# Kernel tuning notes

Hardware: AMD Instinct MI355X
Metric: run time of the kernel (lower is better)

Reference implementation:

```python
import jax, jax.numpy as jnp
import numpy as np

BETA = 0.1


def setup_inputs() -> dict:
    key = jax.random.key(0)
    ks = jax.random.split(key, 8)
    B, S, H, V = 4, 512, 2048, 32000
    return {
        "lin_weight": jax.random.normal(ks[0], (V, H), jnp.float32) * 0.02,
        "_input": jax.random.normal(ks[1], (B, S, H), jnp.float32),
        "attention_mask": jnp.ones((B, S), jnp.float32),
        "rewards": jax.random.normal(ks[2], (B,), jnp.float32),
        "bias": jax.random.normal(ks[3], (V,), jnp.float32) * 0.02,
        "ref_input": jax.random.normal(ks[4], (B, S, H), jnp.float32),
        "ref_weight": jax.random.normal(ks[5], (V, H), jnp.float32) * 0.02,
        "ref_bias": jax.random.normal(ks[6], (V,), jnp.float32) * 0.02,
    }


def _seq_logps(x, w, b, mask):
    # logits: [B,S,V]; per-token max log-softmax, masked, summed over seq
    logits = jnp.einsum("bsh,vh->bsv", x, w) + b
    lp = jax.nn.log_softmax(logits, axis=-1)
    seq = (jnp.max(lp, axis=-1) * mask).sum(axis=-1)  # [B]
    return logits, seq


def reference(lin_weight, _input, attention_mask, rewards, bias, ref_input, ref_weight, ref_bias):
    policy_logits, seq_log_probs = _seq_logps(_input, lin_weight, bias, attention_mask)
    _, ref_seq_logps = _seq_logps(ref_input, ref_weight, ref_bias, attention_mask)
    ref_seq_logps = jax.lax.stop_gradient(ref_seq_logps)

    adv = rewards - rewards.mean()
    std = jnp.std(rewards, ddof=1)  # torch unbiased std
    adv = jnp.where(std > 0, adv / std, adv)

    kl_div = seq_log_probs - ref_seq_logps
    loss = (-(adv * seq_log_probs) + BETA * kl_div).mean()

    metrics = (
        seq_log_probs.mean(),
        jnp.std(seq_log_probs, ddof=1),
        policy_logits.mean(),
        kl_div.mean(),
    )
    return (loss,) + metrics
```

## Files before the change

kernel.cpp:

```cpp
#include <hip/hip_runtime.h>
#include <hip/hip_fp16.h>
#include <math.h>

#define TOK 2048
#define HD 2048
#define VOC 32000
#define BM 256
#define BN 256
#define BK 64
#define NT (HD/BK)
#define NCH (VOC/64)
#define NBLK ((TOK/BM)*(VOC/BN))

typedef _Float16 half8 __attribute__((ext_vector_type(8)));
typedef float float4v __attribute__((ext_vector_type(4)));

#define GLB __attribute__((address_space(1)))
#define LDSAS __attribute__((address_space(3)))

static __device__ __forceinline__ void gload_lds16(const void* g, void* l) {
  __builtin_amdgcn_global_load_lds((const GLB unsigned int*)g,
                                   (LDSAS unsigned int*)l, 16, 0, 0);
}

__global__ void cvt_f32_f16(const float* __restrict__ in,
                            _Float16* __restrict__ out, int n8) {
  for (int i = blockIdx.x * blockDim.x + threadIdx.x; i < n8;
       i += gridDim.x * blockDim.x) {
    float4v a = *(const float4v*)(in + (size_t)i*8);
    float4v b = *(const float4v*)(in + (size_t)i*8 + 4);
    half8 h;
    #pragma unroll
    for (int j=0;j<4;j++) { h[j] = (_Float16)a[j]; h[4+j] = (_Float16)b[j]; }
    *(half8*)(out + (size_t)i*8) = h;
  }
}

template<int CB, bool SG01, bool SG23, int VMN>
__device__ __forceinline__ void ktile(
    unsigned char* ldsby, const char* Xb, const char* Wb,
    int sA0, int sA1, int sB0, int sB1, int ldst0, int ldst1, int kbn,
    const int (&aofs)[2][8], const int (&bofs)[2][4], float4v (&acc)[8][4])
{
  constexpr int BI = CB ? 1 : 0;
  half8 af[4], bf[4];

  #pragma unroll
  for (int m=0;m<4;m++) af[m] = *(const half8*)(ldsby + aofs[BI][m]);
  #pragma unroll
  for (int n=0;n<4;n++) bf[n] = *(const half8*)(ldsby + bofs[BI][n] + 16384);
  if (SG01) {
    gload_lds16(Xb + (sA0 + kbn + 64), ldsby + ((CB^65536) + 32768) + ldst0);
    gload_lds16(Xb + (sA1 + kbn + 64), ldsby + ((CB^65536) + 32768) + ldst1);
  }
  __builtin_amdgcn_s_barrier();
  asm volatile("s_waitcnt lgkmcnt(0)" ::: "memory");
  __builtin_amdgcn_sched_barrier(0);
  __builtin_amdgcn_s_setprio(1);
  #pragma unroll
  for (int m=0;m<4;m++)
    #pragma unroll
    for (int n=0;n<4;n++)
      acc[m][n] = __builtin_amdgcn_mfma_f32_16x16x32_f16(af[m], bf[n], acc[m][n],0,0,0);
  __builtin_amdgcn_s_setprio(0);
  __builtin_amdgcn_s_barrier();

  #pragma unroll
  for (int m=0;m<4;m++) af[m] = *(const half8*)(ldsby + aofs[BI][4+m]);
  if (SG01) {
    gload_lds16(Wb + (sB0 + kbn + 64), ldsby + ((CB^65536) + 49152) + ldst0);
    gload_lds16(Wb + (sB1 + kbn + 64), ldsby + ((CB^65536) + 49152) + ldst1);
  }
  __builtin_amdgcn_s_barrier();
  asm volatile("s_waitcnt lgkmcnt(0)" ::: "memory");
  __builtin_amdgcn_sched_barrier(0);
  __builtin_amdgcn_s_setprio(1);
  #pragma unroll
  for (int m=0;m<4;m++)
    #pragma unroll
    for (int n=0;n<4;n++)
      acc[4+m][n] = __builtin_amdgcn_mfma_f32_16x16x32_f16(af[m], bf[n], acc[4+m][n],0,0,0);
  __builtin_amdgcn_s_setprio(0);
  __builtin_amdgcn_s_barrier();

  #pragma unroll
  for (int m=0;m<4;m++) af[m] = *(const half8*)(ldsby + aofs[BI][m] + 32768);
  #pragma unroll
  for (int n=0;n<4;n++) bf[n] = *(const half8*)(ldsby + bofs[BI][n] + 49152);
  if (SG23) {
    gload_lds16(Xb + (sA0 + kbn + 128), ldsby + (CB + 0) + ldst0);
    gload_lds16(Xb + (sA1 + kbn + 128), ldsby + (CB + 0) + ldst1);
  }
  __builtin_amdgcn_s_barrier();
  asm volatile("s_waitcnt lgkmcnt(0)" ::: "memory");
  __builtin_amdgcn_sched_barrier(0);
  __builtin_amdgcn_s_setprio(1);
  #pragma unroll
  for (int m=0;m<4;m++)
    #pragma unroll
    for (int n=0;n<4;n++)
      acc[m][n] = __builtin_amdgcn_mfma_f32_16x16x32_f16(af[m], bf[n], acc[m][n],0,0,0);
  __builtin_amdgcn_s_setprio(0);
  __builtin_amdgcn_s_barrier();

  #pragma unroll
  for (int m=0;m<4;m++) af[m] = *(const half8*)(ldsby + aofs[BI][4+m] + 32768);
  if (SG23) {
    gload_lds16(Wb + (sB0 + kbn + 128), ldsby + (CB + 16384) + ldst0);
    gload_lds16(Wb + (sB1 + kbn + 128), ldsby + (CB + 16384) + ldst1);
  }
  __builtin_amdgcn_s_barrier();
  asm volatile("s_waitcnt lgkmcnt(0)" ::: "memory");
  __builtin_amdgcn_sched_barrier(0);
  __builtin_amdgcn_s_setprio(1);
  #pragma unroll
  for (int m=0;m<4;m++)
    #pragma unroll
    for (int n=0;n<4;n++)
      acc[4+m][n] = __builtin_amdgcn_mfma_f32_16x16x32_f16(af[m], bf[n], acc[4+m][n],0,0,0);
  __builtin_amdgcn_s_setprio(0);
  if (VMN >= 0) {
    if (VMN == 4) asm volatile("s_waitcnt vmcnt(4)" ::: "memory");
    else          asm volatile("s_waitcnt vmcnt(0)" ::: "memory");
  }
  __builtin_amdgcn_s_barrier();
}

__global__ __launch_bounds__(512, 2) void gemm_stats_f16(
    const _Float16* __restrict__ Xh, const _Float16* __restrict__ Wh,
    const float* __restrict__ bias,
    float* __restrict__ pmax, float* __restrict__ psum,
    float* __restrict__ bsum, int computeSum)
{
  __shared__ unsigned char ldsbuf[131072];
  unsigned char* ldsby = ldsbuf;

  int bid = blockIdx.x;
  int swz = (bid & 7) * (NBLK/8) + (bid >> 3);
  int rowt = swz & 7;
  int colt = swz >> 3;
  int brow = rowt * BM;
  int bcol = colt * BN;

  int tid  = threadIdx.x;
  int lane = tid & 63;
  int wv   = tid >> 6;
  int wr   = wv >> 2;
  int wc   = wv & 3;
  int l15  = lane & 15;
  int q    = lane >> 4;

  int aofs[2][8], bofs[2][4];
  #pragma unroll
  for (int m = 0; m < 8; m++) {
    int r = wr*128 + m*16 + l15;
    int o = r*64 + (((q + r + (r>>2)) & 3) << 4);
    aofs[0][m] = o; aofs[1][m] = o + 65536;
  }
  #pragma unroll
  for (int n = 0; n < 4; n++) {
    int r = wc*64 + n*16 + l15;
    int o = r*64 + (((q + r + (r>>2)) & 3) << 4);
    bofs[0][n] = o; bofs[1][n] = o + 65536;
  }

  int r0 = tid >> 2, c0 = tid & 3;
  int r1 = r0 + 128;
  int q0 = (c0 - r0 - (r0>>2)) & 3;
  int q1 = (c0 - r1 - (r1>>2)) & 3;
  int sA0 = (brow + r0)*(HD*2) + (q0<<4);
  int sA1 = (brow + r1)*(HD*2) + (q1<<4);
  int sB0 = (bcol + r0)*(HD*2) + (q0<<4);
  int sB1 = (bcol + r1)*(HD*2) + (q1<<4);
  int ldst0 = (wv<<10);
  int ldst1 = (wv<<10) + 8192;

  const char* Xb = (const char*)Xh;
  const char* Wb = (const char*)Wh;

  float4v acc[8][4];
  #pragma unroll
  for (int m=0;m<8;m++)
    #pragma unroll
    for (int n=0;n<4;n++) acc[m][n] = (float4v){0.f,0.f,0.f,0.f};

  gload_lds16(Xb + sA0,       ldsby + 0     + ldst0);
  gload_lds16(Xb + sA1,       ldsby + 0     + ldst1);
  gload_lds16(Wb + sB0,       ldsby + 16384 + ldst0);
  gload_lds16(Wb + sB1,       ldsby + 16384 + ldst1);
  gload_lds16(Xb + (sA0+64),  ldsby + 32768 + ldst0);
  gload_lds16(Xb + (sA1+64),  ldsby + 32768 + ldst1);
  gload_lds16(Wb + (sB0+64),  ldsby + 49152 + ldst0);
  gload_lds16(Wb + (sB1+64),  ldsby + 49152 + ldst1);
  gload_lds16(Xb + (sA0+128), ldsby + 65536 + ldst0);
  gload_lds16(Xb + (sA1+128), ldsby + 65536 + ldst1);
  gload_lds16(Wb + (sB0+128), ldsby + 81920 + ldst0);
  gload_lds16(Wb + (sB1+128), ldsby + 81920 + ldst1);
  asm volatile("s_waitcnt vmcnt(4)" ::: "memory");
  __builtin_amdgcn_s_barrier();

  int kbn = 128;
  #pragma unroll 1
  for (int i = 0; i < 15; ++i) {
    ktile<0,     true, true, 4>(ldsby, Xb, Wb, sA0,sA1,sB0,sB1, ldst0,ldst1, kbn, aofs, bofs, acc);
    kbn += 128;
    ktile<65536, true, true, 4>(ldsby, Xb, Wb, sA0,sA1,sB0,sB1, ldst0,ldst1, kbn, aofs, bofs, acc);
    kbn += 128;
  }
  ktile<0,     true,  false, 0>(ldsby, Xb, Wb, sA0,sA1,sB0,sB1, ldst0,ldst1, kbn, aofs, bofs, acc);
  kbn += 128;
  ktile<65536, false, false, -2>(ldsby, Xb, Wb, sA0,sA1,sB0,sB1, ldst0,ldst1, kbn, aofs, bofs, acc);

  float bv[4];
  #pragma unroll
  for (int n=0;n<4;n++) bv[n] = bias[bcol + wc*64 + n*16 + l15];

  float lsum = 0.f;
  int ch = colt*4 + wc;
  #pragma unroll
  for (int m=0;m<8;m++) {
    #pragma unroll
    for (int r=0;r<4;r++) {
      float v0 = acc[m][0][r] + bv[0];
      float v1 = acc[m][1][r] + bv[1];
      float v2 = acc[m][2][r] + bv[2];
      float v3 = acc[m][3][r] + bv[3];
      if (computeSum) lsum += v0+v1+v2+v3;
      float mx = fmaxf(fmaxf(v0,v1), fmaxf(v2,v3));
      #pragma unroll
      for (int off=1; off<16; off<<=1) mx = fmaxf(mx, __shfl_xor(mx, off, 64));
      float se = __expf(v0-mx)+__expf(v1-mx)+__expf(v2-mx)+__expf(v3-mx);
      #pragma unroll
      for (int off=1; off<16; off<<=1) se += __shfl_xor(se, off, 64);
      if (l15 == 0) {
        int row = brow + wr*128 + m*16 + (lane>>4)*4 + r;
        pmax[(size_t)row*NCH + ch] = mx;
        psum[(size_t)row*NCH + ch] = se;
      }
    }
  }

  if (computeSum) {
    #pragma unroll
    for (int off=1; off<64; off<<=1) lsum += __shfl_xor(lsum, off, 64);
    __syncthreads();
    float* red = (float*)ldsbuf;
    if (lane == 0) red[wv] = lsum;
    __syncthreads();
    if (tid == 0) {
      float s = 0.f;
      for (int w=0; w<8; w++) s += red[w];
      bsum[blockIdx.x] = s;
    }
  }
}

__global__ void row_combine(const float* __restrict__ pmax,
                            const float* __restrict__ psum,
                            const float* __restrict__ mask,
                            float* __restrict__ tok)
{
  int row = blockIdx.x;
  int lane = threadIdx.x;
  float M = -INFINITY;
  for (int c = lane; c < NCH; c += 64) M = fmaxf(M, pmax[(size_t)row*NCH + c]);
  #pragma unroll
  for (int off=1; off<64; off<<=1) M = fmaxf(M, __shfl_xor(M, off, 64));
  float L = 0.f;
  for (int c = lane; c < NCH; c += 64)
    L += psum[(size_t)row*NCH + c] * __expf(pmax[(size_t)row*NCH + c] - M);
  #pragma unroll
  for (int off=1; off<64; off<<=1) L += __shfl_xor(L, off, 64);
  if (lane == 0) tok[row] = -logf(L) * mask[row];
}

__global__ void finalize(const float* __restrict__ tokP,
                         const float* __restrict__ tokR,
                         const float* __restrict__ rewards,
                         const float* __restrict__ bsum, int nbsum,
                         float* __restrict__ out)
{
  __shared__ float red[256];
  __shared__ float seqP[4], seqR[4];
  int t = threadIdx.x;
  for (int b=0; b<4; b++) {
    float v = tokP[b*512 + t] + tokP[b*512 + 256 + t];
    red[t] = v; __syncthreads();
    for (int s=128; s>0; s>>=1) { if (t < s) red[t] += red[t+s]; __syncthreads(); }
    if (t == 0) seqP[b] = red[0];
    __syncthreads();
    v = tokR[b*512 + t] + tokR[b*512 + 256 + t];
    red[t] = v; __syncthreads();
    for (int s=128; s>0; s>>=1) { if (t < s) red[t] += red[t+s]; __syncthreads(); }
    if (t == 0) seqR[b] = red[0];
    __syncthreads();
  }
  float ls = 0.f;
  for (int i=t; i<nbsum; i+=256) ls += bsum[i];
  red[t] = ls; __syncthreads();
  for (int s=128; s>0; s>>=1) { if (t < s) red[t] += red[t+s]; __syncthreads(); }
  if (t == 0) {
    float r0=rewards[0], r1=rewards[1], r2=rewards[2], r3=rewards[3];
    float rm = (r0+r1+r2+r3)*0.25f;
    float var = ((r0-rm)*(r0-rm)+(r1-rm)*(r1-rm)+(r2-rm)*(r2-rm)+(r3-rm)*(r3-rm))/3.f;
    float rstd = sqrtf(var);
    float adv[4] = {r0-rm, r1-rm, r2-rm, r3-rm};
    if (rstd > 0.f) { for (int b=0;b<4;b++) adv[b] /= rstd; }
    float loss=0.f, sm=0.f, km=0.f;
    for (int b=0;b<4;b++) {
      float kl = seqP[b] - seqR[b];
      loss += -(adv[b]*seqP[b]) + 0.1f*kl;
      sm += seqP[b]; km += kl;
    }
    loss *= 0.25f; sm *= 0.25f; km *= 0.25f;
    float sv = 0.f;
    for (int b=0;b<4;b++) { float d = seqP[b]-sm; sv += d*d; }
    float sstd = sqrtf(sv/3.f);
    out[0] = loss;
    out[1] = sm;
    out[2] = sstd;
    out[3] = red[0] / ((float)TOK * (float)VOC);
    out[4] = km;
  }
}

extern "C" void kernel_launch(void* const* d_in, const int* in_sizes, int n_in,
                              void* d_out, int out_size, void* d_ws, size_t ws_size,
                              hipStream_t stream) {
  const float* W    = (const float*)d_in[0];
  const float* X    = (const float*)d_in[1];
  const float* mask = (const float*)d_in[2];
  const float* rew  = (const float*)d_in[3];
  const float* bias = (const float*)d_in[4];
  const float* Xr   = (const float*)d_in[5];
  const float* Wr   = (const float*)d_in[6];
  const float* br   = (const float*)d_in[7];
  float* out = (float*)d_out;

  float* pmax = (float*)d_ws;
  float* psum = pmax + (size_t)TOK*NCH;
  float* tokP = psum + (size_t)TOK*NCH;
  float* tokR = tokP + TOK;
  float* bsum = tokR + TOK;

  size_t headFloats = (size_t)TOK*NCH*2 + TOK*2 + 4096;
  size_t offXh = headFloats * 4;
  _Float16* Xh = (_Float16*)((unsigned char*)d_ws + offXh);
  _Float16* Wh = (_Float16*)((unsigned char*)d_ws + offXh + (size_t)TOK*HD*2);

  cvt_f32_f16<<<2048, 256, 0, stream>>>(X,  Xh, TOK*HD/8);
  cvt_f32_f16<<<2048, 256, 0, stream>>>(W,  Wh, VOC*HD/8);
  gemm_stats_f16<<<NBLK, 512, 0, stream>>>(Xh, Wh, bias, pmax, psum, bsum, 1);
  row_combine<<<TOK, 64, 0, stream>>>(pmax, psum, mask, tokP);
  cvt_f32_f16<<<2048, 256, 0, stream>>>(Xr, Xh, TOK*HD/8);
  cvt_f32_f16<<<2048, 256, 0, stream>>>(Wr, Wh, VOC*HD/8);
  gemm_stats_f16<<<NBLK, 512, 0, stream>>>(Xh, Wh, br, pmax, psum, bsum, 0);
  row_combine<<<TOK, 64, 0, stream>>>(pmax, psum, mask, tokR);
  finalize<<<1, 256, 0, stream>>>(tokP, tokR, rew, bsum, NBLK, out);
}
```

Baseline: 718.1 us.

## Merge k-tile GEMM phases into two and overlap LDS reads with MFMAs

Each 128-wide k-step of the fused GEMM now runs in two phases instead of four. All eight A fragments are read from LDS at once, and each phase issues both the X and W prefetches into the other buffer. A partial `lgkmcnt(4)` wait lets the first half of the MFMAs start while the remaining LDS reads are still in flight. This cuts the number of workgroup barriers per k-step and the idle time around them, at the cost of 16 more VGPRs for the extra A fragments, which could raise register pressure under the 512-thread, 2-block launch bound.

```diff
diff --git a/kernel.cpp b/kernel.cpp
--- a/kernel.cpp
+++ b/kernel.cpp
@@ -36,29 +36,37 @@
   }
 }
 
-template<int CB, bool SG01, bool SG23, int VMN>
+template<int CB, bool SG1, bool SG2, int VMN>
 __device__ __forceinline__ void ktile(
     unsigned char* ldsby, const char* Xb, const char* Wb,
     int sA0, int sA1, int sB0, int sB1, int ldst0, int ldst1, int kbn,
     const int (&aofs)[2][8], const int (&bofs)[2][4], float4v (&acc)[8][4])
 {
   constexpr int BI = CB ? 1 : 0;
-  half8 af[4], bf[4];
-
-  #pragma unroll
-  for (int m=0;m<4;m++) af[m] = *(const half8*)(ldsby + aofs[BI][m]);
+  half8 af[8], bf[4];
+
   #pragma unroll
   for (int n=0;n<4;n++) bf[n] = *(const half8*)(ldsby + bofs[BI][n] + 16384);
-  if (SG01) {
+  #pragma unroll
+  for (int m=0;m<8;m++) af[m] = *(const half8*)(ldsby + aofs[BI][m]);
+  if (SG1) {
     gload_lds16(Xb + (sA0 + kbn + 64), ldsby + ((CB^65536) + 32768) + ldst0);
     gload_lds16(Xb + (sA1 + kbn + 64), ldsby + ((CB^65536) + 32768) + ldst1);
-  }
-  __builtin_amdgcn_s_barrier();
+    gload_lds16(Wb + (sB0 + kbn + 64), ldsby + ((CB^65536) + 49152) + ldst0);
+    gload_lds16(Wb + (sB1 + kbn + 64), ldsby + ((CB^65536) + 49152) + ldst1);
+  }
+  asm volatile("s_waitcnt lgkmcnt(4)" ::: "memory");
+  __builtin_amdgcn_sched_barrier(0);
+  __builtin_amdgcn_s_setprio(1);
+  #pragma unroll
+  for (int m=0;m<4;m++)
+    #pragma unroll
+    for (int n=0;n<4;n++)
+      acc[m][n] = __builtin_amdgcn_mfma_f32_16x16x32_f16(af[m], bf[n], acc[m][n],0,0,0);
   asm volatile("s_waitcnt lgkmcnt(0)" ::: "memory");
   __builtin_amdgcn_sched_barrier(0);
-  __builtin_amdgcn_s_setprio(1);
-  #pragma unroll
-  for (int m=0;m<4;m++)
+  #pragma unroll
+  for (int m=4;m<8;m++)
     #pragma unroll
     for (int n=0;n<4;n++)
       acc[m][n] = __builtin_amdgcn_mfma_f32_16x16x32_f16(af[m], bf[n], acc[m][n],0,0,0);
@@ -66,63 +74,33 @@
   __builtin_amdgcn_s_barrier();
 
   #pragma unroll
-  for (int m=0;m<4;m++) af[m] = *(const half8*)(ldsby + aofs[BI][4+m]);
-  if (SG01) {
-    gload_lds16(Wb + (sB0 + kbn + 64), ldsby + ((CB^65536) + 49152) + ldst0);
-    gload_lds16(Wb + (sB1 + kbn + 64), ldsby + ((CB^65536) + 49152) + ldst1);
-  }
-  __builtin_amdgcn_s_barrier();
+  for (int n=0;n<4;n++) bf[n] = *(const half8*)(ldsby + bofs[BI][n] + 49152);
+  #pragma unroll
+  for (int m=0;m<8;m++) af[m] = *(const half8*)(ldsby + aofs[BI][m] + 32768);
+  if (SG2) {
+    gload_lds16(Xb + (sA0 + kbn + 128), ldsby + (CB + 0)     + ldst0);
+    gload_lds16(Xb + (sA1 + kbn + 128), ldsby + (CB + 0)     + ldst1);
+    gload_lds16(Wb + (sB0 + kbn + 128), ldsby + (CB + 16384) + ldst0);
+    gload_lds16(Wb + (sB1 + kbn + 128), ldsby + (CB + 16384) + ldst1);
+  }
+  asm volatile("s_waitcnt lgkmcnt(4)" ::: "memory");
+  __builtin_amdgcn_sched_barrier(0);
+  __builtin_amdgcn_s_setprio(1);
+  #pragma unroll
+  for (int m=0;m<4;m++)
+    #pragma unroll
+    for (int n=0;n<4;n++)
+      acc[m][n] = __builtin_amdgcn_mfma_f32_16x16x32_f16(af[m], bf[n], acc[m][n],0,0,0);
   asm volatile("s_waitcnt lgkmcnt(0)" ::: "memory");
   __builtin_amdgcn_sched_barrier(0);
-  __builtin_amdgcn_s_setprio(1);
-  #pragma unroll
-  for (int m=0;m<4;m++)
-    #pragma unroll
-    for (int n=0;n<4;n++)
-      acc[4+m][n] = __builtin_amdgcn_mfma_f32_16x16x32_f16(af[m], bf[n], acc[4+m][n],0,0,0);
-  __builtin_amdgcn_s_setprio(0);
-  __builtin_amdgcn_s_barrier();
-
-  #pragma unroll
-  for (int m=0;m<4;m++) af[m] = *(const half8*)(ldsby + aofs[BI][m] + 32768);
-  #pragma unroll
-  for (int n=0;n<4;n++) bf[n] = *(const half8*)(ldsby + bofs[BI][n] + 49152);
-  if (SG23) {
-    gload_lds16(Xb + (sA0 + kbn + 128), ldsby + (CB + 0) + ldst0);
-    gload_lds16(Xb + (sA1 + kbn + 128), ldsby + (CB + 0) + ldst1);
-  }
-  __builtin_amdgcn_s_barrier();
-  asm volatile("s_waitcnt lgkmcnt(0)" ::: "memory");
-  __builtin_amdgcn_sched_barrier(0);
-  __builtin_amdgcn_s_setprio(1);
-  #pragma unroll
-  for (int m=0;m<4;m++)
+  #pragma unroll
+  for (int m=4;m<8;m++)
     #pragma unroll
     for (int n=0;n<4;n++)
       acc[m][n] = __builtin_amdgcn_mfma_f32_16x16x32_f16(af[m], bf[n], acc[m][n],0,0,0);
   __builtin_amdgcn_s_setprio(0);
-  __builtin_amdgcn_s_barrier();
-
-  #pragma unroll
-  for (int m=0;m<4;m++) af[m] = *(const half8*)(ldsby + aofs[BI][4+m] + 32768);
-  if (SG23) {
-    gload_lds16(Wb + (sB0 + kbn + 128), ldsby + (CB + 16384) + ldst0);
-    gload_lds16(Wb + (sB1 + kbn + 128), ldsby + (CB + 16384) + ldst1);
-  }
-  __builtin_amdgcn_s_barrier();
-  asm volatile("s_waitcnt lgkmcnt(0)" ::: "memory");
-  __builtin_amdgcn_sched_barrier(0);
-  __builtin_amdgcn_s_setprio(1);
-  #pragma unroll
-  for (int m=0;m<4;m++)
-    #pragma unroll
-    for (int n=0;n<4;n++)
-      acc[4+m][n] = __builtin_amdgcn_mfma_f32_16x16x32_f16(af[m], bf[n], acc[4+m][n],0,0,0);
-  __builtin_amdgcn_s_setprio(0);
-  if (VMN >= 0) {
-    if (VMN == 4) asm volatile("s_waitcnt vmcnt(4)" ::: "memory");
-    else          asm volatile("s_waitcnt vmcnt(0)" ::: "memory");
-  }
+  if (VMN == 4)      asm volatile("s_waitcnt vmcnt(4)" ::: "memory");
+  else if (VMN == 0) asm volatile("s_waitcnt vmcnt(0)" ::: "memory");
   __builtin_amdgcn_s_barrier();
 }
 
@@ -209,7 +187,7 @@
   }
   ktile<0,     true,  false, 0>(ldsby, Xb, Wb, sA0,sA1,sB0,sB1, ldst0,ldst1, kbn, aofs, bofs, acc);
   kbn += 128;
-  ktile<65536, false, false, -2>(ldsby, Xb, Wb, sA0,sA1,sB0,sB1, ldst0,ldst1, kbn, aofs, bofs, acc);
+  ktile<65536, false, false, -1>(ldsby, Xb, Wb, sA0,sA1,sB0,sB1, ldst0,ldst1, kbn, aofs, bofs, acc);
 
   float bv[4];
   #pragma unroll
```

Measured after the change: 706.2 us. Within noise of the previous version (-1.7%).
